# Kernel tuning notes

Hardware: AMD Instinct MI355X
Metric: run time of the kernel (lower is better)

## Reference

```python
import jax, jax.numpy as jnp
import numpy as np

NODE_TYPES = ('user', 'vn', 'tag', 'staff', 'producer', 'character', 'trait')
N = {'user': 100000, 'vn': 40000, 'tag': 3000, 'staff': 20000, 'producer': 8000, 'character': 60000, 'trait': 3000}
# (src_type, dst_type) per edge type, in HGATConfig.edge_types order
EDGE_TYPES = (('user','vn'), ('vn','user'), ('vn','tag'), ('tag','vn'), ('vn','staff'), ('staff','vn'),
              ('vn','staff'), ('staff','vn'), ('vn','producer'), ('producer','vn'), ('vn','character'),
              ('character','vn'), ('character','trait'), ('trait','character'))
E_COUNTS = (1000000, 1000000, 500000, 500000, 200000, 200000, 200000, 200000, 100000, 100000, 300000, 300000, 400000, 400000)
HID = 128
LAYERS = 3
# number of edge types targeting each node type (HeteroConv aggr='mean' divisor)
NUM_DST = {'user': 1, 'vn': 6, 'tag': 1, 'staff': 2, 'producer': 1, 'character': 2, 'trait': 1}


def _l2norm(x):
    n = jnp.linalg.norm(x, axis=-1, keepdims=True)
    return x / jnp.maximum(n, 1e-12)


def _layernorm(x, g, b):
    m = jnp.mean(x, axis=-1, keepdims=True)
    v = jnp.mean((x - m) ** 2, axis=-1, keepdims=True)
    return (x - m) * jax.lax.rsqrt(v + 1e-5) * g + b


def _forward(xs, Wp, bp, Wl, bl, Wr, ln_g, ln_b, Wu, bu, Wv, bv, eis):
    # input projection per node type
    h = {t: xs[t] @ Wp[i].T + bp[i] for i, t in enumerate(NODE_TYPES)}
    # inverse in-degree per edge type (constant across layers)
    inv_deg = []
    for e, (st, dt) in enumerate(EDGE_TYPES):
        dst = eis[e][1]
        deg = jax.ops.segment_sum(jnp.ones(dst.shape[0], jnp.float32), dst, num_segments=N[dt])
        inv_deg.append(1.0 / jnp.maximum(deg, 1.0))
    for l in range(LAYERS):
        acc = {t: jnp.zeros((N[t], HID), h[t].dtype) for t in NODE_TYPES}
        for e, (st, dt) in enumerate(EDGE_TYPES):
            src, dst = eis[e][0], eis[e][1]
            # SAGEConv: mean-aggregate neighbor feats, then lin_l(agg) + lin_r(root), L2-normalize
            agg = jax.ops.segment_sum(h[st][src], dst, num_segments=N[dt]) * inv_deg[e][:, None]
            out = agg @ Wl[l, e].T + bl[l, e] + h[dt] @ Wr[l, e].T
            acc[dt] = acc[dt] + _l2norm(out)
        new_h = {}
        for i, t in enumerate(NODE_TYPES):
            x = acc[t] / NUM_DST[t] + h[t]  # HeteroConv mean over edge types + residual
            new_h[t] = jax.nn.relu(_layernorm(x, ln_g[l, i], ln_b[l, i]))  # dropout = identity (eval)
        h = new_h
    user_emb = _l2norm(h['user'] @ Wu.T + bu)
    vn_emb = _l2norm(h['vn'] @ Wv.T + bv)
    return user_emb, vn_emb


def setup_inputs() -> dict:
    key = jax.random.key(0)
    ks = iter(jax.random.split(key, 80))
    inp = {}
    for t in NODE_TYPES:
        inp['x_' + t] = jax.random.normal(next(ks), (N[t], HID), jnp.float32)
    for e, (st, dt) in enumerate(EDGE_TYPES):
        src = jax.random.randint(next(ks), (E_COUNTS[e],), 0, N[st], jnp.int32)
        dst = jax.random.randint(next(ks), (E_COUNTS[e],), 0, N[dt], jnp.int32)
        inp['ei_%d' % e] = jnp.stack([src, dst])
    s = 1.0 / np.sqrt(HID)
    inp['Wp'] = jax.random.normal(next(ks), (7, HID, HID), jnp.float32) * s
    inp['bp'] = jnp.zeros((7, HID), jnp.float32)
    inp['Wl'] = jax.random.normal(next(ks), (LAYERS, 14, HID, HID), jnp.float32) * s
    inp['bl'] = jnp.zeros((LAYERS, 14, HID), jnp.float32)
    inp['Wr'] = jax.random.normal(next(ks), (LAYERS, 14, HID, HID), jnp.float32) * s
    inp['ln_g'] = jnp.ones((LAYERS, 7, HID), jnp.float32)
    inp['ln_b'] = jnp.zeros((LAYERS, 7, HID), jnp.float32)
    inp['Wu'] = jax.random.normal(next(ks), (HID, HID), jnp.float32) * s
    inp['bu'] = jnp.zeros((HID,), jnp.float32)
    inp['Wv'] = jax.random.normal(next(ks), (HID, HID), jnp.float32) * s
    inp['bv'] = jnp.zeros((HID,), jnp.float32)
    return inp


def reference(x_user, x_vn, x_tag, x_staff, x_producer, x_character, x_trait,
              ei_0, ei_1, ei_2, ei_3, ei_4, ei_5, ei_6, ei_7, ei_8, ei_9, ei_10, ei_11, ei_12, ei_13,
              Wp, bp, Wl, bl, Wr, ln_g, ln_b, Wu, bu, Wv, bv):
    xs = {'user': x_user, 'vn': x_vn, 'tag': x_tag, 'staff': x_staff,
          'producer': x_producer, 'character': x_character, 'trait': x_trait}
    eis = [ei_0, ei_1, ei_2, ei_3, ei_4, ei_5, ei_6, ei_7, ei_8, ei_9, ei_10, ei_11, ei_12, ei_13]
    return _forward(xs, Wp, bp, Wl, bl, Wr, ln_g, ln_b, Wu, bu, Wv, bv, eis)
```

## Files before the change

kernel.cpp:

```cpp
#include <hip/hip_runtime.h>
#include <math.h>

#define TOTE 5400000
#define TOTN 234000
#define TOTC 514000
#define HID  128

#define NBUK 499
#define NBLK 1024


typedef __attribute__((ext_vector_type(8))) short short8;
typedef __attribute__((ext_vector_type(8))) __bf16 bf16x8;
typedef __attribute__((ext_vector_type(4))) float floatx4;

__constant__ int c_EPRE[15]   = {0,1000000,2000000,2500000,3000000,3200000,3400000,3600000,3800000,3900000,4000000,4300000,4600000,5000000,5400000};
__constant__ int c_ECNT[14]   = {1000000,1000000,500000,500000,200000,200000,200000,200000,100000,100000,300000,300000,400000,400000};
__constant__ int c_CNTOFF[14] = {0,40000,140000,143000,183000,203000,243000,263000,303000,311000,351000,411000,451000,454000};
__constant__ int c_CNTN[14]   = {40000,100000,3000,40000,20000,40000,20000,40000,8000,40000,60000,40000,3000,60000};
__constant__ int c_SRCOFF[14] = {0,100000,100000,140000,100000,143000,100000,143000,100000,163000,100000,171000,171000,231000};
__constant__ int c_NODEPRE[8] = {0,100000,140000,143000,163000,171000,231000,234000};
__constant__ float c_INVND[7] = {1.0f, 1.0f/6.0f, 1.0f, 0.5f, 1.0f, 0.5f, 1.0f};
__constant__ int c_UPD_NS[7]      = {1,6,1,2,1,2,1};
__constant__ int c_UPD_BASE[7][6] = {
    {40000,0,0,0,0,0},
    {0,143000,203000,263000,311000,411000},
    {140000,0,0,0,0,0},
    {183000,243000,0,0,0,0},
    {303000,0,0,0,0,0},
    {351000,454000,0,0,0,0},
    {451000,0,0,0,0,0}};
__constant__ int c_BSH[14]   = {9,10,6,10,10,11,10,11,10,11,11,11,6,11};
__constant__ int c_BBASE[15] = {0,79,177,224,264,284,304,324,344,352,372,402,422,469,499};

static __device__ __forceinline__ unsigned short f2bf(float f) {
    unsigned u = __float_as_uint(f);
    u = u + 0x7FFFu + ((u >> 16) & 1u);
    return (unsigned short)(u >> 16);
}
static __device__ __forceinline__ float bf2f(unsigned short s) {
    return __uint_as_float(((unsigned)s) << 16);
}
static __device__ __forceinline__ unsigned short f2h(float f) {
    _Float16 h = (_Float16)f;
    return __builtin_bit_cast(unsigned short, h);
}
static __device__ __forceinline__ float h2f(unsigned short s) {
    _Float16 h = __builtin_bit_cast(_Float16, s);
    return (float)h;
}

struct EdgeArgs { const int* ei[14]; };


__global__ __launch_bounds__(256) void hist_k(EdgeArgs a, int* __restrict__ blkHist) {
    __shared__ int h[NBUK];
    int t = threadIdx.x;
    for (int i = t; i < NBUK; i += 256) h[i] = 0;
    __syncthreads();
    const int per = (TOTE + NBLK - 1) / NBLK;
    int s = blockIdx.x * per;
    int eEnd = min(s + per, TOTE);
    for (int g = s + t; g < eEnd; g += 256) {
        int e = 0;
        while (g >= c_EPRE[e + 1]) e++;
        int k = g - c_EPRE[e];
        int dst = a.ei[e][c_ECNT[e] + k];
        atomicAdd(&h[c_BBASE[e] + (dst >> c_BSH[e])], 1);
    }
    __syncthreads();
    for (int i = t; i < NBUK; i += 256) blkHist[(size_t)i * NBLK + blockIdx.x] = h[i];
}

__global__ __launch_bounds__(256) void scan_blk_k(int* __restrict__ blkHist, int* __restrict__ bktCnt) {
    int b = blockIdx.x;
    int* p = blkHist + (size_t)b * NBLK;
    int t = threadIdx.x;
    int4 v = *(int4*)&p[t * 4];
    int s = v.x + v.y + v.z + v.w;
    int lane = t & 63, w = t >> 6;
    __shared__ int wt[4];
    int incl = s;
    #pragma unroll
    for (int d = 1; d < 64; d <<= 1) { int o = __shfl_up(incl, d); if (lane >= d) incl += o; }
    if (lane == 63) wt[w] = incl;
    __syncthreads();
    int wb = 0;
    for (int i = 0; i < w; i++) wb += wt[i];
    int excl = incl - s + wb;
    int4 o;
    o.x = excl; o.y = excl + v.x; o.z = excl + v.x + v.y; o.w = excl + v.x + v.y + v.z;
    *(int4*)&p[t * 4] = o;
    if (t == 255) bktCnt[b] = excl + s;
}

__global__ __launch_bounds__(512) void scans2_k(const int* __restrict__ bktCnt, int* __restrict__ bktEdgeBase) {
    int t = threadIdx.x;
    int v = (t < NBUK) ? bktCnt[t] : 0;
    int lane = t & 63, w = t >> 6;
    __shared__ int wt[8];
    int incl = v;
    #pragma unroll
    for (int d = 1; d < 64; d <<= 1) { int o = __shfl_up(incl, d); if (lane >= d) incl += o; }
    if (lane == 63) wt[w] = incl;
    __syncthreads();
    int wb = 0;
    for (int i = 0; i < w; i++) wb += wt[i];
    int excl = incl - v + wb;
    if (t < NBUK) bktEdgeBase[t] = excl;
    if (t == NBUK - 1) bktEdgeBase[NBUK] = excl + v;
}

__global__ __launch_bounds__(256) void scatter_k(EdgeArgs a, const int* __restrict__ blkHist,
        const int* __restrict__ bktEdgeBase, unsigned* __restrict__ pool) {
    __shared__ int cur[NBUK];
    int t = threadIdx.x;
    for (int i = t; i < NBUK; i += 256)
        cur[i] = bktEdgeBase[i] + blkHist[(size_t)i * NBLK + blockIdx.x];
    __syncthreads();
    const int per = (TOTE + NBLK - 1) / NBLK;
    int s = blockIdx.x * per;
    int eEnd = min(s + per, TOTE);
    for (int g = s + t; g < eEnd; g += 256) {
        int e = 0;
        while (g >= c_EPRE[e + 1]) e++;
        int k = g - c_EPRE[e];
        int src = a.ei[e][k];
        int dst = a.ei[e][c_ECNT[e] + k];
        int sh = c_BSH[e];
        unsigned rec = ((unsigned)(dst & ((1 << sh) - 1)) << 18) | (unsigned)(c_SRCOFF[e] + src);
        int p = atomicAdd(&cur[c_BBASE[e] + (dst >> sh)], 1);
        pool[p] = rec;
    }
}

__global__ __launch_bounds__(256) void csrfill_k(
        const unsigned* __restrict__ pool, const int* __restrict__ bktEdgeBase,
        int* __restrict__ cnt, int* __restrict__ cursor, float* __restrict__ invdeg,
        int* __restrict__ col) {
    __shared__ int hist[2048];
    __shared__ int cur[2048];
    __shared__ int wtot[4];
    __shared__ int wbase[4];
    int b = blockIdx.x;
    int t = threadIdx.x;
    int e = 0;
    while (b >= c_BBASE[e + 1]) e++;
    int lb = b - c_BBASE[e];
    int sh = c_BSH[e];
    int s0t = lb << sh;
    int span = min(1 << sh, c_CNTN[e] - s0t);
    int gs0 = c_CNTOFF[e] + s0t;
    int ebase = bktEdgeBase[b];
    int nrec = bktEdgeBase[b + 1] - ebase;

    for (int i = t; i < span; i += 256) hist[i] = 0;
    __syncthreads();
    for (int i = t; i < nrec; i += 256) atomicAdd(&hist[pool[ebase + i] >> 18], 1);
    __syncthreads();
    int base = t * 8, loc = 0, lv[8];
    #pragma unroll
    for (int i = 0; i < 8; i++) {
        int ii = base + i;
        int v = (ii < span) ? hist[ii] : 0;
        lv[i] = loc; loc += v;
    }
    int lane = t & 63, w = t >> 6;
    int incl = loc;
    #pragma unroll
    for (int d = 1; d < 64; d <<= 1) { int o = __shfl_up(incl, d); if (lane >= d) incl += o; }
    if (lane == 63) wtot[w] = incl;
    __syncthreads();
    if (t == 0) { int s2 = 0; for (int i = 0; i < 4; i++) { wbase[i] = s2; s2 += wtot[i]; } }
    __syncthreads();
    int texcl = incl - loc + wbase[w];
    #pragma unroll
    for (int i = 0; i < 8; i++) {
        int ii = base + i;
        if (ii < span) cur[ii] = texcl + lv[i];
    }
    __syncthreads();
    for (int i = t; i < span; i += 256) {
        int c = hist[i];
        cnt[gs0 + i] = c;
        cursor[gs0 + i] = ebase + cur[i] + c;
        invdeg[gs0 + i] = 1.0f / fmaxf((float)c, 1.0f);
    }
    __syncthreads();
    for (int i = t; i < nrec; i += 256) {
        unsigned rec = pool[ebase + i];
        int p = atomicAdd(&cur[rec >> 18], 1);
        col[ebase + p] = (int)(rec & 0x3FFFFu);
    }
}

struct XArgs { const float* x[7]; };
__global__ __launch_bounds__(256) void convx_k(XArgs a, unsigned short* __restrict__ hbf) {
    int i4 = blockIdx.x * 256 + threadIdx.x;
    if (i4 >= TOTN * 32) return;
    int idx = i4 * 4;
    int t = 0;
    while (idx >= c_NODEPRE[t + 1] * 128) t++;
    float4 v = *(const float4*)&a.x[t][idx - c_NODEPRE[t] * 128];
    uint2 p;
    p.x = (unsigned)f2bf(v.x) | ((unsigned)f2bf(v.y) << 16);
    p.y = (unsigned)f2bf(v.z) | ((unsigned)f2bf(v.w) << 16);
    *(uint2*)&hbf[idx] = p;
}

struct WArgs { const float* Wp; const float* Wl; const float* Wr; const float* Wu; const float* Wv; };
__global__ __launch_bounds__(256) void convw_k(WArgs a, unsigned short* __restrict__ wbf) {
    int i4 = blockIdx.x * 256 + threadIdx.x;
    if (i4 >= 93 * 4096) return;
    int idx = i4 * 4;
    int m = idx >> 14;
    int i = idx & 16383;
    const float* src;
    if (m < 7)       src = a.Wp + (size_t)m * 16384;
    else if (m < 49) src = a.Wl + (size_t)(m - 7) * 16384;
    else if (m < 91) src = a.Wr + (size_t)(m - 49) * 16384;
    else if (m == 91) src = a.Wu;
    else              src = a.Wv;
    float4 v = *(const float4*)&src[i];
    uint2 p;
    p.x = (unsigned)f2bf(v.x) | ((unsigned)f2bf(v.y) << 16);
    p.y = (unsigned)f2bf(v.z) | ((unsigned)f2bf(v.w) << 16);
    *(uint2*)&wbf[idx] = p;
}

#define ACC8(u) do { \
    v[0] += __uint_as_float((u).x << 16); v[1] += __uint_as_float((u).x & 0xFFFF0000u); \
    v[2] += __uint_as_float((u).y << 16); v[3] += __uint_as_float((u).y & 0xFFFF0000u); \
    v[4] += __uint_as_float((u).z << 16); v[5] += __uint_as_float((u).z & 0xFFFF0000u); \
    v[6] += __uint_as_float((u).w << 16); v[7] += __uint_as_float((u).w & 0xFFFF0000u); } while (0)

__global__ __launch_bounds__(256) void agg_k(
        const int* __restrict__ cnt, const int* __restrict__ cursor,
        const float* __restrict__ inv_deg, const int* __restrict__ col,
        const unsigned short* __restrict__ hbf, unsigned short* __restrict__ slotb) {
    int row = blockIdx.x * 4 + (threadIdx.x >> 6);
    if (row >= TOTC) return;
    int lane = threadIdx.x & 63;
    int q = lane >> 4, li = lane & 15;
    int nn = cnt[row];
    int rs = cursor[row] - nn;
    const int* cp = col + rs;
    float v[8];
    #pragma unroll
    for (int i = 0; i < 8; i++) v[i] = 0.f;
    int j = 0;
    for (; j + 8 <= nn; j += 8) {
        int c0 = cp[j + q] << 7;
        int c1 = cp[j + 4 + q] << 7;
        uint4 u0 = *(const uint4*)&hbf[c0 + li * 8];
        uint4 u1 = *(const uint4*)&hbf[c1 + li * 8];
        ACC8(u0);
        ACC8(u1);
    }
    for (; j < nn; j += 4) {
        if (j + q < nn) {
            int c = cp[j + q] << 7;
            uint4 u = *(const uint4*)&hbf[c + li * 8];
            ACC8(u);
        }
    }
    float inv = inv_deg[row];
    #pragma unroll
    for (int i = 0; i < 8; i++) {
        v[i] += __shfl_xor(v[i], 16);
        v[i] += __shfl_xor(v[i], 32);
        v[i] *= inv;
    }
    if (q == 0) {
        uint4 o;
        o.x = (unsigned)f2bf(v[0]) | ((unsigned)f2bf(v[1]) << 16);
        o.y = (unsigned)f2bf(v[2]) | ((unsigned)f2bf(v[3]) << 16);
        o.z = (unsigned)f2bf(v[4]) | ((unsigned)f2bf(v[5]) << 16);
        o.w = (unsigned)f2bf(v[6]) | ((unsigned)f2bf(v[7]) << 16);
        *(uint4*)&slotb[(size_t)row * HID + li * 8] = o;
    }
}

struct GemmArgs {
    int blockPrefix[15];
    const unsigned short* A1[14]; const unsigned short* A2[14];
    const unsigned short* W1[14]; const unsigned short* W2[14];
    const float* bias[14]; void* out[14];
    int rows[14];
};

template<int MODE, bool TWO>
__global__ __launch_bounds__(256) void gemm_k(GemmArgs g) {
    __shared__ short As[64 * 40];
    __shared__ short Ws[128 * 40];
    int b = blockIdx.x;
    int s = 0;
    while (b >= g.blockPrefix[s + 1]) s++;
    int rows = g.rows[s];
    int row0 = (b - g.blockPrefix[s]) * 64;
    int t = threadIdx.x;
    int w = t >> 6, lane = t & 63;
    int q = lane >> 4, m15 = lane & 15;

    floatx4 acc[8];
    #pragma unroll
    for (int bb = 0; bb < 8; bb++) acc[bb] = (floatx4){0.f, 0.f, 0.f, 0.f};

    const int MM = TWO ? 2 : 1;
    for (int mm = 0; mm < MM; mm++) {
        const uint4* A4 = (const uint4*)(mm ? g.A2[s] : g.A1[s]);
        const uint4* W4 = (const uint4*)(mm ? g.W2[s] : g.W1[s]);
        for (int k0 = 0; k0 < 128; k0 += 32) {
            __syncthreads();
            {
                int row = t >> 2, kc = t & 3;
                uint4 v = make_uint4(0u, 0u, 0u, 0u);
                if (row0 + row < rows) v = A4[(size_t)(row0 + row) * 16 + (k0 >> 3) + kc];
                *(uint4*)&As[row * 40 + kc * 8] = v;
            }
            #pragma unroll
            for (int i = 0; i < 2; i++) {
                int idx = t + i * 256;
                int c = idx >> 2, kc = idx & 3;
                uint4 v = W4[(size_t)c * 16 + (k0 >> 3) + kc];
                *(uint4*)&Ws[c * 40 + kc * 8] = v;
            }
            __syncthreads();
            bf16x8 af = __builtin_bit_cast(bf16x8, *(const short8*)&As[(w * 16 + m15) * 40 + q * 8]);
            #pragma unroll
            for (int bb = 0; bb < 8; bb++) {
                bf16x8 bf = __builtin_bit_cast(bf16x8, *(const short8*)&Ws[(bb * 16 + m15) * 40 + q * 8]);
                acc[bb] = __builtin_amdgcn_mfma_f32_16x16x32_bf16(af, bf, acc[bb], 0, 0, 0);
            }
        }
    }

    const float* bias = g.bias[s];
    #pragma unroll
    for (int bb = 0; bb < 8; bb++) {
        float bv = bias[bb * 16 + m15];
        #pragma unroll
        for (int reg = 0; reg < 4; reg++) acc[bb][reg] += bv;
    }
    if (MODE != 0) {
        #pragma unroll
        for (int reg = 0; reg < 4; reg++) {
            float ss = 0.f;
            #pragma unroll
            for (int bb = 0; bb < 8; bb++) ss += acc[bb][reg] * acc[bb][reg];
            ss += __shfl_xor(ss, 1);
            ss += __shfl_xor(ss, 2);
            ss += __shfl_xor(ss, 4);
            ss += __shfl_xor(ss, 8);
            float sc = 1.0f / fmaxf(sqrtf(ss), 1e-12f);
            #pragma unroll
            for (int bb = 0; bb < 8; bb++) acc[bb][reg] *= sc;
        }
    }
    int rbase = row0 + w * 16 + q * 4;
    if (MODE == 3) {
        float* out = (float*)g.out[s];
        #pragma unroll
        for (int reg = 0; reg < 4; reg++) {
            int r = rbase + reg;
            if (r < rows) {
                float* o = out + (size_t)r * HID;
                #pragma unroll
                for (int bb = 0; bb < 8; bb++) o[bb * 16 + m15] = acc[bb][reg];
            }
        }
    } else {
        unsigned short* out = (unsigned short*)g.out[s];
        #pragma unroll
        for (int reg = 0; reg < 4; reg++) {
            int r = rbase + reg;
            if (r < rows) {
                unsigned short* o = out + (size_t)r * HID;
                #pragma unroll
                for (int bb = 0; bb < 8; bb++)
                    o[bb * 16 + m15] = (MODE == 0) ? f2bf(acc[bb][reg]) : f2h(acc[bb][reg]);
            }
        }
    }
}

__global__ __launch_bounds__(256) void update_k(unsigned short* __restrict__ hbf,
                                                const unsigned short* __restrict__ slotb,
                                                const float* __restrict__ ln_g, const float* __restrict__ ln_b, int l) {
    int row = blockIdx.x * 4 + (threadIdx.x >> 6);
    if (row >= TOTN) return;
    int lane = threadIdx.x & 63;
    int t = 0;
    while (row >= c_NODEPRE[t + 1]) t++;
    int r = row - c_NODEPRE[t];
    int ns = c_UPD_NS[t];
    float s0 = 0.f, s1 = 0.f;
    for (int s = 0; s < ns; s++) {
        const unsigned short* sp = slotb + (size_t)(c_UPD_BASE[t][s] + r) * HID;
        s0 += h2f(sp[lane]);
        s1 += h2f(sp[lane + 64]);
    }
    float invnd = c_INVND[t];
    const float* gg = ln_g + ((size_t)l * 7 + t) * HID;
    const float* bb = ln_b + ((size_t)l * 7 + t) * HID;
    unsigned short* hp = hbf + (size_t)row * HID;
    float x0 = s0 * invnd + bf2f(hp[lane]);
    float x1 = s1 * invnd + bf2f(hp[lane + 64]);
    float s = x0 + x1;
    s += __shfl_xor(s, 1);  s += __shfl_xor(s, 2);  s += __shfl_xor(s, 4);
    s += __shfl_xor(s, 8);  s += __shfl_xor(s, 16); s += __shfl_xor(s, 32);
    float mean = s * (1.0f / 128.0f);
    float d0 = x0 - mean, d1 = x1 - mean;
    float vs = d0 * d0 + d1 * d1;
    vs += __shfl_xor(vs, 1);  vs += __shfl_xor(vs, 2);  vs += __shfl_xor(vs, 4);
    vs += __shfl_xor(vs, 8);  vs += __shfl_xor(vs, 16); vs += __shfl_xor(vs, 32);
    float rstd = rsqrtf(vs * (1.0f / 128.0f) + 1e-5f);
    float y0 = d0 * rstd * gg[lane]      + bb[lane];
    float y1 = d1 * rstd * gg[lane + 64] + bb[lane + 64];
    hp[lane]      = f2bf(fmaxf(y0, 0.f));
    hp[lane + 64] = f2bf(fmaxf(y1, 0.f));
}

extern "C" void kernel_launch(void* const* d_in, const int* in_sizes, int n_in,
                              void* d_out, int out_size, void* d_ws, size_t ws_size,
                              hipStream_t stream) {
    (void)in_sizes; (void)n_in; (void)out_size; (void)ws_size;
    const float* Wp   = (const float*)d_in[21];
    const float* bp   = (const float*)d_in[22];
    const float* Wl   = (const float*)d_in[23];
    const float* bl   = (const float*)d_in[24];
    const float* Wr   = (const float*)d_in[25];
    const float* ln_g = (const float*)d_in[26];
    const float* ln_b = (const float*)d_in[27];
    const float* Wu   = (const float*)d_in[28];
    const float* bu   = (const float*)d_in[29];
    const float* Wv   = (const float*)d_in[30];
    const float* bv   = (const float*)d_in[31];
    float* out = (float*)d_out;

    unsigned short* h_bf   = (unsigned short*)d_ws;
    unsigned short* w_bf   = h_bf + (size_t)TOTN * HID;
    unsigned short* slotb  = w_bf + (size_t)93 * 16384;
    int*            cnt    = (int*)(slotb + (size_t)TOTC * HID);
    int*            cursor = cnt + TOTC;
    float*          invdeg = (float*)(cursor + TOTC);
    unsigned*       pool   = (unsigned*)(invdeg + TOTC);
    int*            blkHist = (int*)(pool + (size_t)TOTE);
    int*            ctrl    = blkHist + (size_t)NBUK * NBLK;
    int* bktCnt       = ctrl;
    int* bktEdgeBase  = ctrl + NBUK;

    int* col = (int*)d_out;

    static const int CNTOFF[14] = {0,40000,140000,143000,183000,203000,243000,263000,303000,311000,351000,411000,451000,454000};
    static const int CNTN[14]   = {40000,100000,3000,40000,20000,40000,20000,40000,8000,40000,60000,40000,3000,60000};
    static const int DSTOFF[14] = {100000,0,140000,100000,143000,100000,143000,100000,163000,100000,171000,100000,231000,171000};
    static const int NODEPRE[8] = {0,100000,140000,143000,163000,171000,231000,234000};
    static const int NT[7]      = {100000,40000,3000,20000,8000,60000,3000};

    EdgeArgs ea;
    for (int e = 0; e < 14; e++) ea.ei[e] = (const int*)d_in[7 + e];

    hist_k<<<NBLK, 256, 0, stream>>>(ea, blkHist);
    scan_blk_k<<<NBUK, 256, 0, stream>>>(blkHist, bktCnt);
    scans2_k<<<1, 512, 0, stream>>>(bktCnt, bktEdgeBase);
    scatter_k<<<NBLK, 256, 0, stream>>>(ea, blkHist, bktEdgeBase, pool);
    csrfill_k<<<NBUK, 256, 0, stream>>>(pool, bktEdgeBase, cnt, cursor, invdeg, col);

    {
        XArgs xa;
        for (int t = 0; t < 7; t++) xa.x[t] = (const float*)d_in[t];
        convx_k<<<(TOTN * 32 + 255) / 256, 256, 0, stream>>>(xa, h_bf);
        WArgs wa = {Wp, Wl, Wr, Wu, Wv};
        convw_k<<<(93 * 4096 + 255) / 256, 256, 0, stream>>>(wa, w_bf);
    }

    {
        GemmArgs ga;
        int pre = 0; ga.blockPrefix[0] = 0;
        for (int t = 0; t < 7; t++) {
            ga.A1[t] = h_bf + (size_t)NODEPRE[t] * HID;
            ga.A2[t] = nullptr;
            ga.W1[t] = w_bf + (size_t)t * 16384;
            ga.W2[t] = nullptr;
            ga.bias[t] = bp + (size_t)t * HID;
            ga.out[t] = h_bf + (size_t)NODEPRE[t] * HID;
            ga.rows[t] = NT[t];
            pre += (NT[t] + 63) / 64;
            ga.blockPrefix[t + 1] = pre;
        }
        for (int s = 7; s < 14; s++) { ga.blockPrefix[s + 1] = pre; ga.rows[s] = 0; }
        gemm_k<0, false><<<pre, 256, 0, stream>>>(ga);
    }

    int ggrid;
    GemmArgs gl;
    {
        int pre = 0; gl.blockPrefix[0] = 0;
        for (int e = 0; e < 14; e++) {
            gl.rows[e] = CNTN[e];
            pre += (CNTN[e] + 63) / 64;
            gl.blockPrefix[e + 1] = pre;
        }
        ggrid = pre;
    }
    for (int l = 0; l < 3; l++) {
        agg_k<<<(TOTC + 3) / 4, 256, 0, stream>>>(cnt, cursor, invdeg, col, h_bf, slotb);
        for (int e = 0; e < 14; e++) {
            gl.A1[e]   = slotb + (size_t)CNTOFF[e] * HID;
            gl.A2[e]   = h_bf + (size_t)DSTOFF[e] * HID;
            gl.W1[e]   = w_bf + (size_t)(7  + l * 14 + e) * 16384;
            gl.W2[e]   = w_bf + (size_t)(49 + l * 14 + e) * 16384;
            gl.bias[e] = bl + ((size_t)l * 14 + e) * HID;
            gl.out[e]  = slotb + (size_t)CNTOFF[e] * HID;
        }
        gemm_k<1, true><<<ggrid, 256, 0, stream>>>(gl);
        update_k<<<(TOTN + 3) / 4, 256, 0, stream>>>(h_bf, slotb, ln_g, ln_b, l);
    }

    {
        GemmArgs ga;
        ga.blockPrefix[0] = 0;
        ga.A1[0] = h_bf;                        ga.A2[0] = nullptr;
        ga.W1[0] = w_bf + (size_t)91 * 16384;   ga.W2[0] = nullptr;
        ga.bias[0] = bu;                        ga.out[0] = out;
        ga.rows[0] = 100000;
        ga.blockPrefix[1] = (100000 + 63) / 64;
        ga.A1[1] = h_bf + (size_t)100000 * HID; ga.A2[1] = nullptr;
        ga.W1[1] = w_bf + (size_t)92 * 16384;   ga.W2[1] = nullptr;
        ga.bias[1] = bv;                        ga.out[1] = out + (size_t)100000 * HID;
        ga.rows[1] = 40000;
        int tot = ga.blockPrefix[1] + (40000 + 63) / 64;
        for (int s = 2; s < 14; s++) { ga.blockPrefix[s + 1] = tot; ga.rows[s] = 0; }
        ga.blockPrefix[2] = tot;
        gemm_k<3, false><<<tot, 256, 0, stream>>>(ga);
    }
}
```

Before: 1.613 ms.

## Fuse neighbor aggregation with SAGE linear GEMM and L2 normalization per layer

Merges the per-layer gather-mean aggregation kernel into the dual GEMM kernel. Each block aggregates 64 destination rows into shared memory, then multiplies them with W_l and the root features with W_r, using weights held in registers. Bias and row-wise L2 normalization are applied before writing fp16 results. This removes the aggregated-feature round trip through global memory and one launch per layer. In exchange, the gather phase now runs with fewer, larger blocks (64 rows each), which may hurt latency hiding, and it uses more shared memory per block.

```diff
diff --git a/kernel.cpp b/kernel.cpp
--- a/kernel.cpp
+++ b/kernel.cpp
@@ -228,68 +228,169 @@
     *(uint2*)&wbf[idx] = p;
 }
 
+
 #define ACC8(u) do { \
     v[0] += __uint_as_float((u).x << 16); v[1] += __uint_as_float((u).x & 0xFFFF0000u); \
     v[2] += __uint_as_float((u).y << 16); v[3] += __uint_as_float((u).y & 0xFFFF0000u); \
     v[4] += __uint_as_float((u).z << 16); v[5] += __uint_as_float((u).z & 0xFFFF0000u); \
     v[6] += __uint_as_float((u).w << 16); v[7] += __uint_as_float((u).w & 0xFFFF0000u); } while (0)
 
-__global__ __launch_bounds__(256) void agg_k(
+struct AgArgs {
+    int blockPrefix[15];
+    const unsigned short* W1[14];
+    const unsigned short* W2[14];
+    const float* bias[14];
+    int cntoff[14];
+    int dstoff[14];
+    int rows[14];
+};
+
+__global__ __launch_bounds__(256) void aggemm_k(AgArgs g,
         const int* __restrict__ cnt, const int* __restrict__ cursor,
-        const float* __restrict__ inv_deg, const int* __restrict__ col,
+        const float* __restrict__ inv_deg, const int* __restrict__ colp,
         const unsigned short* __restrict__ hbf, unsigned short* __restrict__ slotb) {
-    int row = blockIdx.x * 4 + (threadIdx.x >> 6);
-    if (row >= TOTC) return;
-    int lane = threadIdx.x & 63;
-    int q = lane >> 4, li = lane & 15;
-    int nn = cnt[row];
-    int rs = cursor[row] - nn;
-    const int* cp = col + rs;
-    float v[8];
-    #pragma unroll
-    for (int i = 0; i < 8; i++) v[i] = 0.f;
-    int j = 0;
-    for (; j + 8 <= nn; j += 8) {
-        int c0 = cp[j + q] << 7;
-        int c1 = cp[j + 4 + q] << 7;
-        uint4 u0 = *(const uint4*)&hbf[c0 + li * 8];
-        uint4 u1 = *(const uint4*)&hbf[c1 + li * 8];
-        ACC8(u0);
-        ACC8(u1);
-    }
-    for (; j < nn; j += 4) {
-        if (j + q < nn) {
-            int c = cp[j + q] << 7;
-            uint4 u = *(const uint4*)&hbf[c + li * 8];
-            ACC8(u);
-        }
-    }
-    float inv = inv_deg[row];
-    #pragma unroll
-    for (int i = 0; i < 8; i++) {
-        v[i] += __shfl_xor(v[i], 16);
-        v[i] += __shfl_xor(v[i], 32);
-        v[i] *= inv;
-    }
-    if (q == 0) {
-        uint4 o;
-        o.x = (unsigned)f2bf(v[0]) | ((unsigned)f2bf(v[1]) << 16);
-        o.y = (unsigned)f2bf(v[2]) | ((unsigned)f2bf(v[3]) << 16);
-        o.z = (unsigned)f2bf(v[4]) | ((unsigned)f2bf(v[5]) << 16);
-        o.w = (unsigned)f2bf(v[6]) | ((unsigned)f2bf(v[7]) << 16);
-        *(uint4*)&slotb[(size_t)row * HID + li * 8] = o;
+    __shared__ short As1[64 * 168];
+    __shared__ float ssp[64][4];
+    int b = blockIdx.x;
+    int s = 0;
+    while (b >= g.blockPrefix[s + 1]) s++;
+    int rows = g.rows[s];
+    int row0 = (b - g.blockPrefix[s]) * 64;
+    int t = threadIdx.x;
+    int wv = t >> 6, lane = t & 63;
+    int q = lane >> 4, m15 = lane & 15;
+    int cntoff = g.cntoff[s];
+    int doff = g.dstoff[s];
+
+    for (int i = 0; i < 16; i++) {
+        int lrow = wv * 16 + i;
+        int srow = row0 + lrow;
+        float v[8];
+        #pragma unroll
+        for (int ii = 0; ii < 8; ii++) v[ii] = 0.f;
+        if (srow < rows) {
+            int grow = cntoff + srow;
+            int nn = cnt[grow];
+            int rs = cursor[grow] - nn;
+            const int* cp = colp + rs;
+            int j = 0;
+            for (; j + 8 <= nn; j += 8) {
+                int c0 = cp[j + q] << 7;
+                int c1 = cp[j + 4 + q] << 7;
+                uint4 u0 = *(const uint4*)&hbf[c0 + m15 * 8];
+                uint4 u1 = *(const uint4*)&hbf[c1 + m15 * 8];
+                ACC8(u0);
+                ACC8(u1);
+            }
+            for (; j < nn; j += 4) {
+                if (j + q < nn) {
+                    int c = cp[j + q] << 7;
+                    uint4 u = *(const uint4*)&hbf[c + m15 * 8];
+                    ACC8(u);
+                }
+            }
+            float inv = inv_deg[grow];
+            #pragma unroll
+            for (int ii = 0; ii < 8; ii++) {
+                v[ii] += __shfl_xor(v[ii], 16);
+                v[ii] += __shfl_xor(v[ii], 32);
+                v[ii] *= inv;
+            }
+        }
+        if (q == 0) {
+            uint4 o;
+            o.x = (unsigned)f2bf(v[0]) | ((unsigned)f2bf(v[1]) << 16);
+            o.y = (unsigned)f2bf(v[2]) | ((unsigned)f2bf(v[3]) << 16);
+            o.z = (unsigned)f2bf(v[4]) | ((unsigned)f2bf(v[5]) << 16);
+            o.w = (unsigned)f2bf(v[6]) | ((unsigned)f2bf(v[7]) << 16);
+            *(uint4*)&As1[lrow * 168 + (m15 >> 2) * 40 + (m15 & 3) * 8] = o;
+        }
+    }
+
+    __builtin_amdgcn_sched_barrier(0);
+    const uint4* W14 = (const uint4*)g.W1[s];
+    const uint4* W24 = (const uint4*)g.W2[s];
+    bf16x8 w1r[2][4], w2r[2][4];
+    #pragma unroll
+    for (int bbl = 0; bbl < 2; bbl++) {
+        int colr = ((2 * wv + bbl) * 16 + m15) * 16;
+        #pragma unroll
+        for (int kc = 0; kc < 4; kc++) {
+            w1r[bbl][kc] = __builtin_bit_cast(bf16x8, W14[colr + kc * 4 + q]);
+            w2r[bbl][kc] = __builtin_bit_cast(bf16x8, W24[colr + kc * 4 + q]);
+        }
+    }
+    __syncthreads();
+
+    const uint4* h4 = (const uint4*)hbf;
+    floatx4 acc[4][2];
+    #pragma unroll
+    for (int m = 0; m < 4; m++) {
+        acc[m][0] = (floatx4){0.f, 0.f, 0.f, 0.f};
+        acc[m][1] = (floatx4){0.f, 0.f, 0.f, 0.f};
+    }
+    #pragma unroll
+    for (int m = 0; m < 4; m++) {
+        int rr = min(row0 + m * 16 + m15, rows - 1);
+        size_t hb = (size_t)(doff + rr) * 16;
+        bf16x8 a2f[4];
+        #pragma unroll
+        for (int kc = 0; kc < 4; kc++) a2f[kc] = __builtin_bit_cast(bf16x8, h4[hb + kc * 4 + q]);
+        #pragma unroll
+        for (int kc = 0; kc < 4; kc++) {
+            bf16x8 a1 = __builtin_bit_cast(bf16x8, *(const short8*)&As1[(m * 16 + m15) * 168 + kc * 40 + q * 8]);
+            acc[m][0] = __builtin_amdgcn_mfma_f32_16x16x32_bf16(a1, w1r[0][kc], acc[m][0], 0, 0, 0);
+            acc[m][1] = __builtin_amdgcn_mfma_f32_16x16x32_bf16(a1, w1r[1][kc], acc[m][1], 0, 0, 0);
+            acc[m][0] = __builtin_amdgcn_mfma_f32_16x16x32_bf16(a2f[kc], w2r[0][kc], acc[m][0], 0, 0, 0);
+            acc[m][1] = __builtin_amdgcn_mfma_f32_16x16x32_bf16(a2f[kc], w2r[1][kc], acc[m][1], 0, 0, 0);
+        }
+    }
+
+    const float* bias = g.bias[s];
+    float bv0 = bias[(2 * wv) * 16 + m15];
+    float bv1 = bias[(2 * wv + 1) * 16 + m15];
+    #pragma unroll
+    for (int m = 0; m < 4; m++) {
+        #pragma unroll
+        for (int reg = 0; reg < 4; reg++) {
+            acc[m][0][reg] += bv0;
+            acc[m][1][reg] += bv1;
+            float ps = acc[m][0][reg] * acc[m][0][reg] + acc[m][1][reg] * acc[m][1][reg];
+            ps += __shfl_xor(ps, 1);
+            ps += __shfl_xor(ps, 2);
+            ps += __shfl_xor(ps, 4);
+            ps += __shfl_xor(ps, 8);
+            if (m15 == 0) ssp[m * 16 + q * 4 + reg][wv] = ps;
+        }
+    }
+    __syncthreads();
+    unsigned short* outp = slotb + (size_t)(cntoff + row0) * HID;
+    #pragma unroll
+    for (int m = 0; m < 4; m++) {
+        #pragma unroll
+        for (int reg = 0; reg < 4; reg++) {
+            int lr = m * 16 + q * 4 + reg;
+            float4 s4 = *(const float4*)&ssp[lr][0];
+            float ss = s4.x + s4.y + s4.z + s4.w;
+            float sc = 1.0f / fmaxf(sqrtf(ss), 1e-12f);
+            if (row0 + lr < rows) {
+                unsigned short* o = outp + (size_t)lr * HID;
+                o[(2 * wv) * 16 + m15]     = f2h(acc[m][0][reg] * sc);
+                o[(2 * wv + 1) * 16 + m15] = f2h(acc[m][1][reg] * sc);
+            }
+        }
     }
 }
 
 struct GemmArgs {
     int blockPrefix[15];
-    const unsigned short* A1[14]; const unsigned short* A2[14];
-    const unsigned short* W1[14]; const unsigned short* W2[14];
+    const unsigned short* A1[14];
+    const unsigned short* W1[14];
     const float* bias[14]; void* out[14];
     int rows[14];
 };
 
-template<int MODE, bool TWO>
+template<int MODE>
 __global__ __launch_bounds__(256) void gemm_k(GemmArgs g) {
     __shared__ short As[64 * 40];
     __shared__ short Ws[128 * 40];
@@ -306,32 +407,29 @@
     #pragma unroll
     for (int bb = 0; bb < 8; bb++) acc[bb] = (floatx4){0.f, 0.f, 0.f, 0.f};
 
-    const int MM = TWO ? 2 : 1;
-    for (int mm = 0; mm < MM; mm++) {
-        const uint4* A4 = (const uint4*)(mm ? g.A2[s] : g.A1[s]);
-        const uint4* W4 = (const uint4*)(mm ? g.W2[s] : g.W1[s]);
-        for (int k0 = 0; k0 < 128; k0 += 32) {
-            __syncthreads();
-            {
-                int row = t >> 2, kc = t & 3;
-                uint4 v = make_uint4(0u, 0u, 0u, 0u);
-                if (row0 + row < rows) v = A4[(size_t)(row0 + row) * 16 + (k0 >> 3) + kc];
-                *(uint4*)&As[row * 40 + kc * 8] = v;
-            }
-            #pragma unroll
-            for (int i = 0; i < 2; i++) {
-                int idx = t + i * 256;
-                int c = idx >> 2, kc = idx & 3;
-                uint4 v = W4[(size_t)c * 16 + (k0 >> 3) + kc];
-                *(uint4*)&Ws[c * 40 + kc * 8] = v;
-            }
-            __syncthreads();
-            bf16x8 af = __builtin_bit_cast(bf16x8, *(const short8*)&As[(w * 16 + m15) * 40 + q * 8]);
-            #pragma unroll
-            for (int bb = 0; bb < 8; bb++) {
-                bf16x8 bf = __builtin_bit_cast(bf16x8, *(const short8*)&Ws[(bb * 16 + m15) * 40 + q * 8]);
-                acc[bb] = __builtin_amdgcn_mfma_f32_16x16x32_bf16(af, bf, acc[bb], 0, 0, 0);
-            }
+    const uint4* A4 = (const uint4*)g.A1[s];
+    const uint4* W4 = (const uint4*)g.W1[s];
+    for (int k0 = 0; k0 < 128; k0 += 32) {
+        __syncthreads();
+        {
+            int row = t >> 2, kc = t & 3;
+            uint4 v = make_uint4(0u, 0u, 0u, 0u);
+            if (row0 + row < rows) v = A4[(size_t)(row0 + row) * 16 + (k0 >> 3) + kc];
+            *(uint4*)&As[row * 40 + kc * 8] = v;
+        }
+        #pragma unroll
+        for (int i = 0; i < 2; i++) {
+            int idx = t + i * 256;
+            int c = idx >> 2, kc = idx & 3;
+            uint4 v = W4[(size_t)c * 16 + (k0 >> 3) + kc];
+            *(uint4*)&Ws[c * 40 + kc * 8] = v;
+        }
+        __syncthreads();
+        bf16x8 af = __builtin_bit_cast(bf16x8, *(const short8*)&As[(w * 16 + m15) * 40 + q * 8]);
+        #pragma unroll
+        for (int bb = 0; bb < 8; bb++) {
+            bf16x8 bf = __builtin_bit_cast(bf16x8, *(const short8*)&Ws[(bb * 16 + m15) * 40 + q * 8]);
+            acc[bb] = __builtin_amdgcn_mfma_f32_16x16x32_bf16(af, bf, acc[bb], 0, 0, 0);
         }
     }
 
@@ -377,8 +475,7 @@
             if (r < rows) {
                 unsigned short* o = out + (size_t)r * HID;
                 #pragma unroll
-                for (int bb = 0; bb < 8; bb++)
-                    o[bb * 16 + m15] = (MODE == 0) ? f2bf(acc[bb][reg]) : f2h(acc[bb][reg]);
+                for (int bb = 0; bb < 8; bb++) o[bb * 16 + m15] = f2bf(acc[bb][reg]);
             }
         }
     }
@@ -480,9 +577,7 @@
         int pre = 0; ga.blockPrefix[0] = 0;
         for (int t = 0; t < 7; t++) {
             ga.A1[t] = h_bf + (size_t)NODEPRE[t] * HID;
-            ga.A2[t] = nullptr;
             ga.W1[t] = w_bf + (size_t)t * 16384;
-            ga.W2[t] = nullptr;
             ga.bias[t] = bp + (size_t)t * HID;
             ga.out[t] = h_bf + (size_t)NODEPRE[t] * HID;
             ga.rows[t] = NT[t];
@@ -490,49 +585,47 @@
             ga.blockPrefix[t + 1] = pre;
         }
         for (int s = 7; s < 14; s++) { ga.blockPrefix[s + 1] = pre; ga.rows[s] = 0; }
-        gemm_k<0, false><<<pre, 256, 0, stream>>>(ga);
-    }
-
-    int ggrid;
-    GemmArgs gl;
+        gemm_k<0><<<pre, 256, 0, stream>>>(ga);
+    }
+
+    int agrid;
+    AgArgs gl;
     {
         int pre = 0; gl.blockPrefix[0] = 0;
         for (int e = 0; e < 14; e++) {
-            gl.rows[e] = CNTN[e];
+            gl.rows[e]   = CNTN[e];
+            gl.cntoff[e] = CNTOFF[e];
+            gl.dstoff[e] = DSTOFF[e];
             pre += (CNTN[e] + 63) / 64;
             gl.blockPrefix[e + 1] = pre;
         }
-        ggrid = pre;
+        agrid = pre;
     }
     for (int l = 0; l < 3; l++) {
-        agg_k<<<(TOTC + 3) / 4, 256, 0, stream>>>(cnt, cursor, invdeg, col, h_bf, slotb);
         for (int e = 0; e < 14; e++) {
-            gl.A1[e]   = slotb + (size_t)CNTOFF[e] * HID;
-            gl.A2[e]   = h_bf + (size_t)DSTOFF[e] * HID;
             gl.W1[e]   = w_bf + (size_t)(7  + l * 14 + e) * 16384;
             gl.W2[e]   = w_bf + (size_t)(49 + l * 14 + e) * 16384;
             gl.bias[e] = bl + ((size_t)l * 14 + e) * HID;
-            gl.out[e]  = slotb + (size_t)CNTOFF[e] * HID;
-        }
-        gemm_k<1, true><<<ggrid, 256, 0, stream>>>(gl);
+        }
+        aggemm_k<<<agrid, 256, 0, stream>>>(gl, cnt, cursor, invdeg, col, h_bf, slotb);
         update_k<<<(TOTN + 3) / 4, 256, 0, stream>>>(h_bf, slotb, ln_g, ln_b, l);
     }
 
     {
         GemmArgs ga;
         ga.blockPrefix[0] = 0;
-        ga.A1[0] = h_bf;                        ga.A2[0] = nullptr;
-        ga.W1[0] = w_bf + (size_t)91 * 16384;   ga.W2[0] = nullptr;
+        ga.A1[0] = h_bf;
+        ga.W1[0] = w_bf + (size_t)91 * 16384;
         ga.bias[0] = bu;                        ga.out[0] = out;
         ga.rows[0] = 100000;
         ga.blockPrefix[1] = (100000 + 63) / 64;
-        ga.A1[1] = h_bf + (size_t)100000 * HID; ga.A2[1] = nullptr;
-        ga.W1[1] = w_bf + (size_t)92 * 16384;   ga.W2[1] = nullptr;
+        ga.A1[1] = h_bf + (size_t)100000 * HID;
+        ga.W1[1] = w_bf + (size_t)92 * 16384;
         ga.bias[1] = bv;                        ga.out[1] = out + (size_t)100000 * HID;
         ga.rows[1] = 40000;
         int tot = ga.blockPrefix[1] + (40000 + 63) / 64;
         for (int s = 2; s < 14; s++) { ga.blockPrefix[s + 1] = tot; ga.rows[s] = 0; }
         ga.blockPrefix[2] = tot;
-        gemm_k<3, false><<<tot, 256, 0, stream>>>(ga);
-    }
-}
+        gemm_k<3><<<tot, 256, 0, stream>>>(ga);
+    }
+}
```

Result: slower. 2.303 ms (+42.8%).

## Add dedicated 128-row dual-operand layer GEMM and prefetch indices in aggregation

Applied to the files above, without the earlier changes.

Replaces the generic two-pass layer GEMM with a specialized kernel that tiles 128 rows per block and stages both operands (aggregated neighbours and root features) plus both weight matrices in shared memory together. It interleaves the two MFMA chains and halves the number of K-loop syncs. This is meant to improve weight reuse and cut per-block overhead, at the cost of more shared memory and registers, which may lower occupancy. The aggregation kernel also software-prefetches the next column indices and accumulates into float2 vectors to hide index-load latency and enable packed adds.

```diff
diff --git a/kernel.cpp b/kernel.cpp
--- a/kernel.cpp
+++ b/kernel.cpp
@@ -13,6 +13,7 @@
 typedef __attribute__((ext_vector_type(8))) short short8;
 typedef __attribute__((ext_vector_type(8))) __bf16 bf16x8;
 typedef __attribute__((ext_vector_type(4))) float floatx4;
+typedef __attribute__((ext_vector_type(2))) float float2v;
 
 __constant__ int c_EPRE[15]   = {0,1000000,2000000,2500000,3000000,3200000,3400000,3600000,3800000,3900000,4000000,4300000,4600000,5000000,5400000};
 __constant__ int c_ECNT[14]   = {1000000,1000000,500000,500000,200000,200000,200000,200000,100000,100000,300000,300000,400000,400000};
@@ -228,11 +229,11 @@
     *(uint2*)&wbf[idx] = p;
 }
 
-#define ACC8(u) do { \
-    v[0] += __uint_as_float((u).x << 16); v[1] += __uint_as_float((u).x & 0xFFFF0000u); \
-    v[2] += __uint_as_float((u).y << 16); v[3] += __uint_as_float((u).y & 0xFFFF0000u); \
-    v[4] += __uint_as_float((u).z << 16); v[5] += __uint_as_float((u).z & 0xFFFF0000u); \
-    v[6] += __uint_as_float((u).w << 16); v[7] += __uint_as_float((u).w & 0xFFFF0000u); } while (0)
+#define ACC8v(u) do { \
+    v01 += (float2v){__uint_as_float((u).x << 16), __uint_as_float((u).x & 0xFFFF0000u)}; \
+    v23 += (float2v){__uint_as_float((u).y << 16), __uint_as_float((u).y & 0xFFFF0000u)}; \
+    v45 += (float2v){__uint_as_float((u).z << 16), __uint_as_float((u).z & 0xFFFF0000u)}; \
+    v67 += (float2v){__uint_as_float((u).w << 16), __uint_as_float((u).w & 0xFFFF0000u)}; } while (0)
 
 __global__ __launch_bounds__(256) void agg_k(
         const int* __restrict__ cnt, const int* __restrict__ cursor,
@@ -245,26 +246,30 @@
     int nn = cnt[row];
     int rs = cursor[row] - nn;
     const int* cp = col + rs;
-    float v[8];
-    #pragma unroll
-    for (int i = 0; i < 8; i++) v[i] = 0.f;
+    float2v v01 = {0.f, 0.f}, v23 = {0.f, 0.f}, v45 = {0.f, 0.f}, v67 = {0.f, 0.f};
     int j = 0;
-    for (; j + 8 <= nn; j += 8) {
-        int c0 = cp[j + q] << 7;
-        int c1 = cp[j + 4 + q] << 7;
-        uint4 u0 = *(const uint4*)&hbf[c0 + li * 8];
-        uint4 u1 = *(const uint4*)&hbf[c1 + li * 8];
-        ACC8(u0);
-        ACC8(u1);
+    if (j + 8 <= nn) {
+        int c0 = cp[q], c1 = cp[4 + q];
+        for (; j + 8 <= nn; ) {
+            int jn = j + 8;
+            int n0 = 0, n1 = 0;
+            if (jn + 8 <= nn) { n0 = cp[jn + q]; n1 = cp[jn + 4 + q]; }
+            uint4 u0 = *(const uint4*)&hbf[(c0 << 7) + li * 8];
+            uint4 u1 = *(const uint4*)&hbf[(c1 << 7) + li * 8];
+            ACC8v(u0);
+            ACC8v(u1);
+            c0 = n0; c1 = n1; j = jn;
+        }
     }
     for (; j < nn; j += 4) {
         if (j + q < nn) {
             int c = cp[j + q] << 7;
             uint4 u = *(const uint4*)&hbf[c + li * 8];
-            ACC8(u);
+            ACC8v(u);
         }
     }
     float inv = inv_deg[row];
+    float v[8] = {v01.x, v01.y, v23.x, v23.y, v45.x, v45.y, v67.x, v67.y};
     #pragma unroll
     for (int i = 0; i < 8; i++) {
         v[i] += __shfl_xor(v[i], 16);
@@ -281,15 +286,123 @@
     }
 }
 
+struct GemmLArgs {
+    int blockPrefix[15];
+    const unsigned short* W1[14];
+    const unsigned short* W2[14];
+    const float* bias[14];
+    int cntoff[14];
+    int dstoff[14];
+    int rows[14];
+};
+
+__global__ __launch_bounds__(256) void gemm_l(GemmLArgs g,
+        const unsigned short* __restrict__ hbf, unsigned short* __restrict__ slotb) {
+    __shared__ short A1s[128 * 40];
+    __shared__ short A2s[128 * 40];
+    __shared__ short W1s[128 * 40];
+    __shared__ short W2s[128 * 40];
+    int b = blockIdx.x;
+    int s = 0;
+    while (b >= g.blockPrefix[s + 1]) s++;
+    int rows = g.rows[s];
+    int row0 = (b - g.blockPrefix[s]) * 128;
+    int t = threadIdx.x;
+    int wv = t >> 6, lane = t & 63;
+    int q = lane >> 4, m15 = lane & 15;
+
+    const uint4* A14 = (const uint4*)(slotb + (size_t)g.cntoff[s] * HID);
+    const uint4* A24 = (const uint4*)(hbf + (size_t)g.dstoff[s] * HID);
+    const uint4* W14 = (const uint4*)g.W1[s];
+    const uint4* W24 = (const uint4*)g.W2[s];
+
+    floatx4 acc[2][8];
+    #pragma unroll
+    for (int m = 0; m < 2; m++)
+        #pragma unroll
+        for (int bb = 0; bb < 8; bb++) acc[m][bb] = (floatx4){0.f, 0.f, 0.f, 0.f};
+
+    for (int k0 = 0; k0 < 4; k0++) {
+        __syncthreads();
+        #pragma unroll
+        for (int i = 0; i < 2; i++) {
+            int idx = t + i * 256;
+            int row = idx >> 2, kc = idx & 3;
+            uint4 va1 = make_uint4(0u, 0u, 0u, 0u), va2 = va1;
+            if (row0 + row < rows) {
+                va1 = A14[(size_t)(row0 + row) * 16 + k0 * 4 + kc];
+                va2 = A24[(size_t)(row0 + row) * 16 + k0 * 4 + kc];
+            }
+            *(uint4*)&A1s[row * 40 + kc * 8] = va1;
+            *(uint4*)&A2s[row * 40 + kc * 8] = va2;
+            uint4 w1 = W14[(size_t)row * 16 + k0 * 4 + kc];
+            uint4 w2 = W24[(size_t)row * 16 + k0 * 4 + kc];
+            *(uint4*)&W1s[row * 40 + kc * 8] = w1;
+            *(uint4*)&W2s[row * 40 + kc * 8] = w2;
+        }
+        __syncthreads();
+        bf16x8 a1[2], a2[2];
+        #pragma unroll
+        for (int m = 0; m < 2; m++) {
+            int r = (wv * 32 + m * 16 + m15) * 40 + q * 8;
+            a1[m] = __builtin_bit_cast(bf16x8, *(const short8*)&A1s[r]);
+            a2[m] = __builtin_bit_cast(bf16x8, *(const short8*)&A2s[r]);
+        }
+        #pragma unroll
+        for (int bb = 0; bb < 8; bb++) {
+            int r = (bb * 16 + m15) * 40 + q * 8;
+            bf16x8 w1 = __builtin_bit_cast(bf16x8, *(const short8*)&W1s[r]);
+            bf16x8 w2 = __builtin_bit_cast(bf16x8, *(const short8*)&W2s[r]);
+            #pragma unroll
+            for (int m = 0; m < 2; m++) {
+                acc[m][bb] = __builtin_amdgcn_mfma_f32_16x16x32_bf16(a1[m], w1, acc[m][bb], 0, 0, 0);
+                acc[m][bb] = __builtin_amdgcn_mfma_f32_16x16x32_bf16(a2[m], w2, acc[m][bb], 0, 0, 0);
+            }
+        }
+    }
+
+    const float* bias = g.bias[s];
+    #pragma unroll
+    for (int bb = 0; bb < 8; bb++) {
+        float bv = bias[bb * 16 + m15];
+        #pragma unroll
+        for (int m = 0; m < 2; m++)
+            #pragma unroll
+            for (int reg = 0; reg < 4; reg++) acc[m][bb][reg] += bv;
+    }
+    unsigned short* outp = slotb + (size_t)g.cntoff[s] * HID;
+    #pragma unroll
+    for (int m = 0; m < 2; m++) {
+        #pragma unroll
+        for (int reg = 0; reg < 4; reg++) {
+            float ss = 0.f;
+            #pragma unroll
+            for (int bb = 0; bb < 8; bb++) ss += acc[m][bb][reg] * acc[m][bb][reg];
+            ss += __shfl_xor(ss, 1);
+            ss += __shfl_xor(ss, 2);
+            ss += __shfl_xor(ss, 4);
+            ss += __shfl_xor(ss, 8);
+            float sc = 1.0f / fmaxf(sqrtf(ss), 1e-12f);
+            int r = row0 + wv * 32 + m * 16 + q * 4 + reg;
+            if (r < rows) {
+                unsigned short* o = outp + (size_t)r * HID;
+                #pragma unroll
+                for (int bb = 0; bb < 8; bb++)
+                    o[bb * 16 + m15] = f2h(acc[m][bb][reg] * sc);
+            }
+        }
+    }
+}
+
 struct GemmArgs {
     int blockPrefix[15];
-    const unsigned short* A1[14]; const unsigned short* A2[14];
-    const unsigned short* W1[14]; const unsigned short* W2[14];
+    const unsigned short* A1[14];
+    const unsigned short* W1[14];
     const float* bias[14]; void* out[14];
     int rows[14];
 };
 
-template<int MODE, bool TWO>
+template<int MODE>
 __global__ __launch_bounds__(256) void gemm_k(GemmArgs g) {
     __shared__ short As[64 * 40];
     __shared__ short Ws[128 * 40];
@@ -306,32 +419,29 @@
     #pragma unroll
     for (int bb = 0; bb < 8; bb++) acc[bb] = (floatx4){0.f, 0.f, 0.f, 0.f};
 
-    const int MM = TWO ? 2 : 1;
-    for (int mm = 0; mm < MM; mm++) {
-        const uint4* A4 = (const uint4*)(mm ? g.A2[s] : g.A1[s]);
-        const uint4* W4 = (const uint4*)(mm ? g.W2[s] : g.W1[s]);
-        for (int k0 = 0; k0 < 128; k0 += 32) {
-            __syncthreads();
-            {
-                int row = t >> 2, kc = t & 3;
-                uint4 v = make_uint4(0u, 0u, 0u, 0u);
-                if (row0 + row < rows) v = A4[(size_t)(row0 + row) * 16 + (k0 >> 3) + kc];
-                *(uint4*)&As[row * 40 + kc * 8] = v;
-            }
-            #pragma unroll
-            for (int i = 0; i < 2; i++) {
-                int idx = t + i * 256;
-                int c = idx >> 2, kc = idx & 3;
-                uint4 v = W4[(size_t)c * 16 + (k0 >> 3) + kc];
-                *(uint4*)&Ws[c * 40 + kc * 8] = v;
-            }
-            __syncthreads();
-            bf16x8 af = __builtin_bit_cast(bf16x8, *(const short8*)&As[(w * 16 + m15) * 40 + q * 8]);
-            #pragma unroll
-            for (int bb = 0; bb < 8; bb++) {
-                bf16x8 bf = __builtin_bit_cast(bf16x8, *(const short8*)&Ws[(bb * 16 + m15) * 40 + q * 8]);
-                acc[bb] = __builtin_amdgcn_mfma_f32_16x16x32_bf16(af, bf, acc[bb], 0, 0, 0);
-            }
+    const uint4* A4 = (const uint4*)g.A1[s];
+    const uint4* W4 = (const uint4*)g.W1[s];
+    for (int k0 = 0; k0 < 128; k0 += 32) {
+        __syncthreads();
+        {
+            int row = t >> 2, kc = t & 3;
+            uint4 v = make_uint4(0u, 0u, 0u, 0u);
+            if (row0 + row < rows) v = A4[(size_t)(row0 + row) * 16 + (k0 >> 3) + kc];
+            *(uint4*)&As[row * 40 + kc * 8] = v;
+        }
+        #pragma unroll
+        for (int i = 0; i < 2; i++) {
+            int idx = t + i * 256;
+            int c = idx >> 2, kc = idx & 3;
+            uint4 v = W4[(size_t)c * 16 + (k0 >> 3) + kc];
+            *(uint4*)&Ws[c * 40 + kc * 8] = v;
+        }
+        __syncthreads();
+        bf16x8 af = __builtin_bit_cast(bf16x8, *(const short8*)&As[(w * 16 + m15) * 40 + q * 8]);
+        #pragma unroll
+        for (int bb = 0; bb < 8; bb++) {
+            bf16x8 bf = __builtin_bit_cast(bf16x8, *(const short8*)&Ws[(bb * 16 + m15) * 40 + q * 8]);
+            acc[bb] = __builtin_amdgcn_mfma_f32_16x16x32_bf16(af, bf, acc[bb], 0, 0, 0);
         }
     }
 
@@ -377,8 +487,7 @@
             if (r < rows) {
                 unsigned short* o = out + (size_t)r * HID;
                 #pragma unroll
-                for (int bb = 0; bb < 8; bb++)
-                    o[bb * 16 + m15] = (MODE == 0) ? f2bf(acc[bb][reg]) : f2h(acc[bb][reg]);
+                for (int bb = 0; bb < 8; bb++) o[bb * 16 + m15] = f2bf(acc[bb][reg]);
             }
         }
     }
@@ -480,9 +589,7 @@
         int pre = 0; ga.blockPrefix[0] = 0;
         for (int t = 0; t < 7; t++) {
             ga.A1[t] = h_bf + (size_t)NODEPRE[t] * HID;
-            ga.A2[t] = nullptr;
             ga.W1[t] = w_bf + (size_t)t * 16384;
-            ga.W2[t] = nullptr;
             ga.bias[t] = bp + (size_t)t * HID;
             ga.out[t] = h_bf + (size_t)NODEPRE[t] * HID;
             ga.rows[t] = NT[t];
@@ -490,49 +597,48 @@
             ga.blockPrefix[t + 1] = pre;
         }
         for (int s = 7; s < 14; s++) { ga.blockPrefix[s + 1] = pre; ga.rows[s] = 0; }
-        gemm_k<0, false><<<pre, 256, 0, stream>>>(ga);
-    }
-
-    int ggrid;
-    GemmArgs gl;
+        gemm_k<0><<<pre, 256, 0, stream>>>(ga);
+    }
+
+    int lgrid;
+    GemmLArgs gl;
     {
         int pre = 0; gl.blockPrefix[0] = 0;
         for (int e = 0; e < 14; e++) {
-            gl.rows[e] = CNTN[e];
-            pre += (CNTN[e] + 63) / 64;
+            gl.rows[e]   = CNTN[e];
+            gl.cntoff[e] = CNTOFF[e];
+            gl.dstoff[e] = DSTOFF[e];
+            pre += (CNTN[e] + 127) / 128;
             gl.blockPrefix[e + 1] = pre;
         }
-        ggrid = pre;
+        lgrid = pre;
     }
     for (int l = 0; l < 3; l++) {
         agg_k<<<(TOTC + 3) / 4, 256, 0, stream>>>(cnt, cursor, invdeg, col, h_bf, slotb);
         for (int e = 0; e < 14; e++) {
-            gl.A1[e]   = slotb + (size_t)CNTOFF[e] * HID;
-            gl.A2[e]   = h_bf + (size_t)DSTOFF[e] * HID;
             gl.W1[e]   = w_bf + (size_t)(7  + l * 14 + e) * 16384;
             gl.W2[e]   = w_bf + (size_t)(49 + l * 14 + e) * 16384;
             gl.bias[e] = bl + ((size_t)l * 14 + e) * HID;
-            gl.out[e]  = slotb + (size_t)CNTOFF[e] * HID;
-        }
-        gemm_k<1, true><<<ggrid, 256, 0, stream>>>(gl);
+        }
+        gemm_l<<<lgrid, 256, 0, stream>>>(gl, h_bf, slotb);
         update_k<<<(TOTN + 3) / 4, 256, 0, stream>>>(h_bf, slotb, ln_g, ln_b, l);
     }
 
     {
         GemmArgs ga;
         ga.blockPrefix[0] = 0;
-        ga.A1[0] = h_bf;                        ga.A2[0] = nullptr;
-        ga.W1[0] = w_bf + (size_t)91 * 16384;   ga.W2[0] = nullptr;
+        ga.A1[0] = h_bf;
+        ga.W1[0] = w_bf + (size_t)91 * 16384;
         ga.bias[0] = bu;                        ga.out[0] = out;
         ga.rows[0] = 100000;
         ga.blockPrefix[1] = (100000 + 63) / 64;
-        ga.A1[1] = h_bf + (size_t)100000 * HID; ga.A2[1] = nullptr;
-        ga.W1[1] = w_bf + (size_t)92 * 16384;   ga.W2[1] = nullptr;
+        ga.A1[1] = h_bf + (size_t)100000 * HID;
+        ga.W1[1] = w_bf + (size_t)92 * 16384;
         ga.bias[1] = bv;                        ga.out[1] = out + (size_t)100000 * HID;
         ga.rows[1] = 40000;
         int tot = ga.blockPrefix[1] + (40000 + 63) / 64;
         for (int s = 2; s < 14; s++) { ga.blockPrefix[s + 1] = tot; ga.rows[s] = 0; }
         ga.blockPrefix[2] = tot;
-        gemm_k<3, false><<<tot, 256, 0, stream>>>(ga);
-    }
-}
+        gemm_k<3><<<tot, 256, 0, stream>>>(ga);
+    }
+}
```

Measured after the change: 1.598 ms. Within noise of the previous version (-1.0%).
